# Kernel tuning notes

Measured on AMD Instinct MI355X. Metric: run time of the kernel, lower is better.

The kernel has to match this reference:

```python
import jax, jax.numpy as jnp
import numpy as np

B, S, D = 8, 1024, 768
H = 12
DH = D // H  # 64
SCALE = 1.0 / (D ** 0.5)  # module scales by full embedding_dim, not head_dim


def setup_inputs() -> dict:
    key = jax.random.key(0)
    ks = jax.random.split(key, 7)
    std = 1.0 / np.sqrt(D)
    return {
        "x": jax.random.normal(ks[0], (B, S, D), dtype=jnp.float32),
        "Wq": jax.random.uniform(ks[1], (D, D), jnp.float32, -std, std),
        "bq": jax.random.uniform(ks[2], (D,), jnp.float32, -std, std),
        "Wk": jax.random.uniform(ks[3], (D, D), jnp.float32, -std, std),
        "bk": jax.random.uniform(ks[4], (D,), jnp.float32, -std, std),
        "Wv": jax.random.uniform(ks[5], (D, D), jnp.float32, -std, std),
        "bv": jax.random.uniform(ks[6], (D,), jnp.float32, -std, std),
    }


def reference(x, Wq, bq, Wk, bk, Wv, bv):
    b, s, d = x.shape
    # projections; torch.chunk(dim=-1) == reshape last dim to [H, DH]
    q = (x @ Wq + bq).reshape(b, s, H, DH)
    k = (x @ Wk + bk).reshape(b, s, H, DH)
    v = (x @ Wv + bv).reshape(b, s, H, DH)
    # per-head scores [b, h, s, s], scaled by sqrt(embedding_dim) per source
    scores = jnp.einsum("bqhd,bkhd->bhqk", q, k) * SCALE
    attn = jax.nn.softmax(scores, axis=-1)
    out = jnp.einsum("bhqk,bkhd->bqhd", attn, v)
    # concat heads back along last dim (order matches chunk order)
    return out.reshape(b, s, d)
```

## Files before the change

kernel.cpp:

```cpp
#include <hip/hip_runtime.h>
#include <cstdint>
#include <cstddef>

typedef unsigned short u16;
typedef unsigned int u32;
typedef unsigned char u8;

using bfx8 = __attribute__((ext_vector_type(8))) __bf16;
using floatx16 = __attribute__((ext_vector_type(16))) float;

static constexpr int kS = 1024;
static constexpr int kD = 768;
static constexpr int kH = 12;
static constexpr int kDH = 64;
#define SCALE 0.036084391824351614f

__device__ __forceinline__ u16 f2bf(float f) {
    u32 u = __float_as_uint(f);
    return (u16)((u + 0x7fffu + ((u >> 16) & 1u)) >> 16);
}

__device__ __forceinline__ void gld16(const void* g, void* l) {
    __builtin_amdgcn_global_load_lds(
        (__attribute__((address_space(1))) const u32*)g,
        (__attribute__((address_space(3))) u32*)l, 16, 0, 0);
}

__global__ __launch_bounds__(256) void cvt_x(const float* __restrict__ x, u16* __restrict__ xb) {
    int i = (blockIdx.x * 256 + threadIdx.x) * 4;
    float4 v = *(const float4*)(x + i);
    u32 lo = (u32)f2bf(v.x) | ((u32)f2bf(v.y) << 16);
    u32 hi = (u32)f2bf(v.z) | ((u32)f2bf(v.w) << 16);
    *(uint2*)(xb + i) = make_uint2(lo, hi);
}

__global__ __launch_bounds__(256) void cvt_w(const float* __restrict__ w0, const float* __restrict__ w1,
                                             const float* __restrict__ w2, u16* __restrict__ wt) {
    __shared__ float t[32][33];
    const float* W = blockIdx.z == 0 ? w0 : (blockIdx.z == 1 ? w1 : w2);
    u16* dst = wt + (size_t)blockIdx.z * kD * kD;
    int k0 = blockIdx.x * 32, n0 = blockIdx.y * 32;
    int tx = threadIdx.x, ty = threadIdx.y;
#pragma unroll
    for (int j = 0; j < 4; j++)
        t[ty + j * 8][tx] = W[(size_t)(k0 + ty + j * 8) * kD + n0 + tx];
    __syncthreads();
#pragma unroll
    for (int j = 0; j < 4; j++)
        dst[(size_t)(n0 + ty + j * 8) * kD + k0 + tx] = f2bf(t[tx][ty + j * 8]);
}

__global__ __launch_bounds__(256) void proj(const u16* __restrict__ xb, const u16* __restrict__ wt,
                                            const float* __restrict__ bq, const float* __restrict__ bk,
                                            const float* __restrict__ bvp,
                                            u16* __restrict__ qb, u16* __restrict__ kb, u16* __restrict__ vt) {
    __shared__ u16 As0[128 * 64];
    __shared__ u16 Bs0[128 * 64];
    __shared__ u16 As1[128 * 64];
    __shared__ u16 Bs1[128 * 64];
    int m0 = blockIdx.x * 128;
    int n0g = blockIdx.y * 128;
    int t = threadIdx.x;
    int w = t >> 6, lane = t & 63;
    int l31 = lane & 31, hi = lane >> 5;
    int wm = (w & 1) * 64, wn = (w >> 1) * 64;
    int rloc8 = lane >> 3, p8 = lane & 7;
    int chw = p8 ^ rloc8;
    const u16* Brow = wt + (size_t)n0g * kD;
    int swz = l31 & 7;
    floatx16 acc[2][2] = {};

    auto STAGE = [&](u16* Ad, u16* Bd, int ks) {
#pragma unroll
        for (int i = 0; i < 4; i++) {
            int j = w * 4 + i;
            int r = 8 * j + rloc8;
            gld16(xb + (size_t)(m0 + r) * kD + ks + chw * 8, Ad + j * 512);
            gld16(Brow + (size_t)r * kD + ks + chw * 8, Bd + j * 512);
        }
    };
    auto COMP = [&](const u16* Ad, const u16* Bd) {
#pragma unroll
        for (int s = 0; s < 4; s++) {
            int tc = ((s * 2 + hi) ^ swz) * 8;
            bfx8 a[2], bf[2];
#pragma unroll
            for (int i = 0; i < 2; i++) {
                a[i] = *(const bfx8*)&Ad[(wm + i * 32 + l31) * 64 + tc];
                bf[i] = *(const bfx8*)&Bd[(wn + i * 32 + l31) * 64 + tc];
            }
#pragma unroll
            for (int i = 0; i < 2; i++)
#pragma unroll
                for (int j2 = 0; j2 < 2; j2++)
                    acc[i][j2] = __builtin_amdgcn_mfma_f32_32x32x16_bf16(a[i], bf[j2], acc[i][j2], 0, 0, 0);
        }
    };

    STAGE(As0, Bs0, 0);
    __syncthreads();
    for (int kk = 0; kk < 5; kk++) {
        STAGE(As1, Bs1, 64 + 128 * kk);
        COMP(As0, Bs0);
        __syncthreads();
        STAGE(As0, Bs0, 128 + 128 * kk);
        COMP(As1, Bs1);
        __syncthreads();
    }
    STAGE(As1, Bs1, 704);
    COMP(As0, Bs0);
    __syncthreads();
    COMP(As1, Bs1);

    int zz = blockIdx.y / 6;
    int nl0 = (blockIdx.y - zz * 6) * 128;
    const float* bias = zz == 0 ? bq : (zz == 1 ? bk : bvp);
    float mul = zz == 0 ? SCALE : 1.0f;
#pragma unroll
    for (int j = 0; j < 2; j++) {
        int nl = nl0 + wn + j * 32 + l31;
        float bb = bias[nl];
#pragma unroll
        for (int i = 0; i < 2; i++) {
            int mbase = m0 + wm + i * 32 + 4 * hi;
            if (zz < 2) {
                u16* dst = zz == 0 ? qb : kb;
#pragma unroll
                for (int reg = 0; reg < 16; reg++) {
                    int m = mbase + (reg & 3) + 8 * (reg >> 2);
                    dst[(size_t)m * kD + nl] = f2bf((acc[i][j][reg] + bb) * mul);
                }
            } else {
                int hh = nl >> 6, dh = nl & 63;
#pragma unroll
                for (int g = 0; g < 4; g++) {
                    int m = (m0 + wm + i * 32) + 4 * (g & 1) + 8 * hi + 16 * (g >> 1);
                    int bi = m >> 10, s = m & 1023;
                    u32 lo = (u32)f2bf(acc[i][j][4 * g + 0] + bb) | ((u32)f2bf(acc[i][j][4 * g + 1] + bb) << 16);
                    u32 h2 = (u32)f2bf(acc[i][j][4 * g + 2] + bb) | ((u32)f2bf(acc[i][j][4 * g + 3] + bb) << 16);
                    *(uint2*)&vt[(((size_t)bi * kH + hh) * kDH + dh) * kS + s] = make_uint2(lo, h2);
                }
            }
        }
    }
}

__global__ __launch_bounds__(256, 3) void attn(const u16* __restrict__ qb, const u16* __restrict__ kb,
                                               const u16* __restrict__ vt, float* __restrict__ out) {
    __shared__ u16 Ks[128 * 64];
    __shared__ u16 Vs[64 * 128];
    __shared__ float Lw[128];
    int q0 = blockIdx.x * 128;
    int bh = blockIdx.y;
    int b = bh / kH, h = bh % kH;
    int t = threadIdx.x, w = t >> 6, lane = t & 63;
    int l31 = lane & 31, hi = lane >> 5;
    int swz = l31 & 7;

    bfx8 qf[4];
    {
        const u16* qrow = qb + (size_t)(b * kS + q0 + w * 32 + l31) * kD + h * kDH + hi * 8;
#pragma unroll
        for (int f = 0; f < 4; f++) qf[f] = *(const bfx8*)(qrow + f * 16);
    }

    float rsum = 0.f;
    floatx16 oacc[2] = {};

    for (int kt = 0; kt < 8; kt++) {
        int kk0 = kt * 128;
        __syncthreads();
#pragma unroll
        for (int i = 0; i < 4; i++) {
            int jj = 4 * w + i;
            int r = 8 * jj + (lane >> 3);
            int c = (lane & 7) ^ ((lane >> 3) & 7);
            gld16(kb + (size_t)(b * kS + kk0 + r) * kD + h * kDH + c * 8, &Ks[jj * 512]);
        }
#pragma unroll
        for (int i = 0; i < 4; i++) {
            int jj = 4 * w + i;
            int r = 4 * jj + (lane >> 4);
            int c = (lane & 15) ^ (r & 15);
            gld16(vt + (((size_t)b * kH + h) * kDH + r) * kS + kk0 + c * 8, &Vs[jj * 512]);
        }
        __syncthreads();

        floatx16 sacc[4] = {};
#pragma unroll
        for (int s2 = 0; s2 < 4; s2++) {
#pragma unroll
            for (int fm = 0; fm < 4; fm++) {
                bfx8 ak = *(const bfx8*)&Ks[(fm * 32 + l31) * 64 + ((s2 * 2 + hi) ^ swz) * 8];
                sacc[fm] = __builtin_amdgcn_mfma_f32_32x32x16_bf16(ak, qf[s2], sacc[fm], 0, 0, 0);
            }
        }

        bfx8 pa[4][2];
#pragma unroll
        for (int fm = 0; fm < 4; fm++) {
#pragma unroll
            for (int hh = 0; hh < 2; hh++) {
                bfx8 pv;
#pragma unroll
                for (int jj = 0; jj < 8; jj++) {
                    float e = __expf(sacc[fm][8 * hh + jj]);
                    rsum += e;
                    pv[jj] = (__bf16)e;
                }
                pa[fm][hh] = pv;
            }
        }

#pragma unroll
        for (int s = 0; s < 8; s++) {
#pragma unroll
            for (int db = 0; db < 2; db++) {
                bfx8 bv = *(const bfx8*)((const u8*)Vs + (db * 32 + l31) * 256 + (((s * 2 + hi) ^ (l31 & 15)) * 16));
                oacc[db] = __builtin_amdgcn_mfma_f32_32x32x16_bf16(pa[s >> 1][s & 1], bv, oacc[db], 0, 0, 0);
            }
        }
    }

    rsum += __shfl_xor(rsum, 32, 64);
    if (lane < 32) Lw[w * 32 + lane] = rsum;
    __syncthreads();
#pragma unroll
    for (int g = 0; g < 4; g++) {
#pragma unroll
        for (int r2 = 0; r2 < 4; r2++) {
            int qloc = w * 32 + 4 * hi + r2 + 8 * g;
            float linv = 1.0f / Lw[qloc];
#pragma unroll
            for (int db = 0; db < 2; db++) {
                out[(size_t)(b * kS + q0 + qloc) * kD + h * kDH + db * 32 + l31] = oacc[db][4 * g + r2] * linv;
            }
        }
    }
}

extern "C" void kernel_launch(void* const* d_in, const int* in_sizes, int n_in,
                              void* d_out, int out_size, void* d_ws, size_t ws_size,
                              hipStream_t stream) {
    const float* x  = (const float*)d_in[0];
    const float* Wq = (const float*)d_in[1];
    const float* bq = (const float*)d_in[2];
    const float* Wk = (const float*)d_in[3];
    const float* bk = (const float*)d_in[4];
    const float* Wv = (const float*)d_in[5];
    const float* bv = (const float*)d_in[6];
    float* out = (float*)d_out;

    u16* ws = (u16*)d_ws;
    u16* xb = ws;
    u16* wt = xb + 6291456;
    u16* qb = wt + 1769472;
    u16* kb = qb + 6291456;
    u16* vt = kb + 6291456;

    cvt_x<<<dim3(6144), dim3(256), 0, stream>>>(x, xb);
    cvt_w<<<dim3(24, 24, 3), dim3(32, 8), 0, stream>>>(Wq, Wk, Wv, wt);
    proj<<<dim3(64, 18), dim3(256), 0, stream>>>(xb, wt, bq, bk, bv, qb, kb, vt);
    attn<<<dim3(8, 96), dim3(256), 0, stream>>>(qb, kb, vt, out);
}
```

Before: 169.9 us.

## Merge conversion kernels and remap workgroups for XCD-local L2 reuse

Merges the x and weight bf16 conversion kernels into one launch, using a block-index split, so one kernel launch and its gap are removed. The projection and attention grids are flattened to 1D, and block IDs are remapped so consecutive IDs within each of the 8 XCDs cover neighbouring tiles. For attention, all query tiles of a (batch, head) then land on the same XCD and share K/V in L2. For projection, tiles that share an x row block are grouped the same way. The remapping assumes round-robin dispatch of blocks across 8 XCDs.

Result: faster. 165.8 us (-2.4%).

```diff
diff --git a/kernel.cpp b/kernel.cpp
--- a/kernel.cpp
+++ b/kernel.cpp
@@ -26,28 +26,34 @@
         (__attribute__((address_space(3))) u32*)l, 16, 0, 0);
 }
 
-__global__ __launch_bounds__(256) void cvt_x(const float* __restrict__ x, u16* __restrict__ xb) {
-    int i = (blockIdx.x * 256 + threadIdx.x) * 4;
-    float4 v = *(const float4*)(x + i);
-    u32 lo = (u32)f2bf(v.x) | ((u32)f2bf(v.y) << 16);
-    u32 hi = (u32)f2bf(v.z) | ((u32)f2bf(v.w) << 16);
-    *(uint2*)(xb + i) = make_uint2(lo, hi);
-}
-
-__global__ __launch_bounds__(256) void cvt_w(const float* __restrict__ w0, const float* __restrict__ w1,
-                                             const float* __restrict__ w2, u16* __restrict__ wt) {
+__global__ __launch_bounds__(256) void cvt(const float* __restrict__ x, u16* __restrict__ xb,
+                                           const float* __restrict__ w0, const float* __restrict__ w1,
+                                           const float* __restrict__ w2, u16* __restrict__ wt) {
     __shared__ float t[32][33];
-    const float* W = blockIdx.z == 0 ? w0 : (blockIdx.z == 1 ? w1 : w2);
-    u16* dst = wt + (size_t)blockIdx.z * kD * kD;
-    int k0 = blockIdx.x * 32, n0 = blockIdx.y * 32;
-    int tx = threadIdx.x, ty = threadIdx.y;
-#pragma unroll
-    for (int j = 0; j < 4; j++)
-        t[ty + j * 8][tx] = W[(size_t)(k0 + ty + j * 8) * kD + n0 + tx];
-    __syncthreads();
-#pragma unroll
-    for (int j = 0; j < 4; j++)
-        dst[(size_t)(n0 + ty + j * 8) * kD + k0 + tx] = f2bf(t[tx][ty + j * 8]);
+    int bid = blockIdx.x;
+    if (bid < 6144) {
+        int i = (bid * 256 + threadIdx.x) * 4;
+        float4 v = *(const float4*)(x + i);
+        u32 lo = (u32)f2bf(v.x) | ((u32)f2bf(v.y) << 16);
+        u32 hi = (u32)f2bf(v.z) | ((u32)f2bf(v.w) << 16);
+        *(uint2*)(xb + i) = make_uint2(lo, hi);
+    } else {
+        int idx = bid - 6144;
+        int z = idx / 576;
+        int rem = idx - z * 576;
+        int by = rem / 24, bx = rem - by * 24;
+        const float* W = z == 0 ? w0 : (z == 1 ? w1 : w2);
+        u16* dst = wt + (size_t)z * kD * kD;
+        int k0 = bx * 32, n0 = by * 32;
+        int tx = threadIdx.x & 31, ty = threadIdx.x >> 5;
+#pragma unroll
+        for (int j = 0; j < 4; j++)
+            t[ty + j * 8][tx] = W[(size_t)(k0 + ty + j * 8) * kD + n0 + tx];
+        __syncthreads();
+#pragma unroll
+        for (int j = 0; j < 4; j++)
+            dst[(size_t)(n0 + ty + j * 8) * kD + k0 + tx] = f2bf(t[tx][ty + j * 8]);
+    }
 }
 
 __global__ __launch_bounds__(256) void proj(const u16* __restrict__ xb, const u16* __restrict__ wt,
@@ -58,8 +64,11 @@
     __shared__ u16 Bs0[128 * 64];
     __shared__ u16 As1[128 * 64];
     __shared__ u16 Bs1[128 * 64];
-    int m0 = blockIdx.x * 128;
-    int n0g = blockIdx.y * 128;
+    int orig = blockIdx.x;
+    int wg = (orig & 7) * 144 + (orig >> 3);
+    int mt = wg / 18, nt = wg - mt * 18;
+    int m0 = mt * 128;
+    int n0g = nt * 128;
     int t = threadIdx.x;
     int w = t >> 6, lane = t & 63;
     int l31 = lane & 31, hi = lane >> 5;
@@ -112,8 +121,8 @@
     __syncthreads();
     COMP(As1, Bs1);
 
-    int zz = blockIdx.y / 6;
-    int nl0 = (blockIdx.y - zz * 6) * 128;
+    int zz = nt / 6;
+    int nl0 = (nt - zz * 6) * 128;
     const float* bias = zz == 0 ? bq : (zz == 1 ? bk : bvp);
     float mul = zz == 0 ? SCALE : 1.0f;
 #pragma unroll
@@ -150,8 +159,10 @@
     __shared__ u16 Ks[128 * 64];
     __shared__ u16 Vs[64 * 128];
     __shared__ float Lw[128];
-    int q0 = blockIdx.x * 128;
-    int bh = blockIdx.y;
+    int orig = blockIdx.x;
+    int wg = (orig & 7) * 96 + (orig >> 3);
+    int bh = wg >> 3;
+    int q0 = (wg & 7) * 128;
     int b = bh / kH, h = bh % kH;
     int t = threadIdx.x, w = t >> 6, lane = t & 63;
     int l31 = lane & 31, hi = lane >> 5;
@@ -258,8 +269,7 @@
     u16* kb = qb + 6291456;
     u16* vt = kb + 6291456;
 
-    cvt_x<<<dim3(6144), dim3(256), 0, stream>>>(x, xb);
-    cvt_w<<<dim3(24, 24, 3), dim3(32, 8), 0, stream>>>(Wq, Wk, Wv, wt);
-    proj<<<dim3(64, 18), dim3(256), 0, stream>>>(xb, wt, bq, bk, bv, qb, kb, vt);
-    attn<<<dim3(8, 96), dim3(256), 0, stream>>>(qb, kb, vt, out);
-}
+    cvt<<<dim3(7872), dim3(256), 0, stream>>>(x, xb, Wq, Wk, Wv, wt);
+    proj<<<dim3(1152), dim3(256), 0, stream>>>(xb, wt, bq, bk, bv, qb, kb, vt);
+    attn<<<dim3(768), dim3(256), 0, stream>>>(qb, kb, vt, out);
+}
```
